# Kernel tuning notes

Measured on AMD Instinct MI355X. Metric: run time of the kernel, lower is better.

Reference implementation:

```python
import jax, jax.numpy as jnp
import numpy as np

N, F, C, E = 1024, 64, 4, 32768
H = 256       # MLP hidden width
C_OUT = 4     # new edge channels produced by nn_edge


def setup_inputs() -> dict:
    key = jax.random.key(0)
    ks = jax.random.split(key, 12)
    x = jax.random.normal(ks[0], (N, F), dtype=jnp.float32)
    edge_index = jax.random.randint(ks[1], (C, 2, E), 0, N)
    edge_weight = jax.random.uniform(ks[2], (C, E), dtype=jnp.float32)
    s_n1 = 1.0 / np.sqrt(C * F)
    s_n2 = 1.0 / np.sqrt(H)
    s_e1 = 1.0 / np.sqrt(C + 2 * F)
    return {
        "x": x,
        "edge_index": edge_index,
        "edge_weight": edge_weight,
        "Wn1": jax.random.normal(ks[3], (C * F, H), dtype=jnp.float32) * s_n1,
        "bn1": jnp.zeros((H,), jnp.float32),
        "Wn2": jax.random.normal(ks[4], (H, F), dtype=jnp.float32) * s_n2,
        "bn2": jnp.zeros((F,), jnp.float32),
        "We1": jax.random.normal(ks[5], (C + 2 * F, H), dtype=jnp.float32) * s_e1,
        "be1": jnp.zeros((H,), jnp.float32),
        "We2": jax.random.normal(ks[6], (H, C_OUT), dtype=jnp.float32) * s_n2,
        "be2": jnp.zeros((C_OUT,), jnp.float32),
        "eps": jnp.zeros((), jnp.float32),
    }


def reference(x, edge_index, edge_weight, Wn1, bn1, Wn2, bn2, We1, be1, We2, be2, eps):
    # ---- MCGNN: per-channel edge-weighted scatter-add aggregation ----
    def agg_one(ei, w):
        # ei: [2,E] (row0 = source j, row1 = target i); w: [E]
        msg = x[ei[0]] * w[:, None]                       # [E,F]
        return jax.ops.segment_sum(msg, ei[1], num_segments=N)  # [N,F]

    agg = jax.vmap(agg_one)(edge_index, edge_weight)      # [C,N,F]
    out_cat = agg + (1.0 + eps) * x                       # broadcast self term
    h = out_cat.transpose(1, 0, 2).reshape(N, C * F)      # [N, C*F]
    x_next = jax.nn.relu(h @ Wn1 + bn1) @ Wn2 + bn2       # [N,F]

    # ---- EDPGNN: dense adjacency per channel + broadcast x_i/x_j ----
    def dense_adj(ei, w):
        return jnp.zeros((N, N), x.dtype).at[ei[0], ei[1]].add(w)

    a = jax.vmap(dense_adj)(edge_index, edge_weight)      # [C,N,N]
    a = a.transpose(1, 2, 0)                              # [N,N,C]
    x_i = jnp.broadcast_to(x_next[:, None, :], (N, N, F))
    x_j = jnp.broadcast_to(x_next[None, :, :], (N, N, F))
    feat = jnp.concatenate([a, x_i, x_j], axis=2).reshape(N * N, C + 2 * F)
    adj_out = (jax.nn.relu(feat @ We1 + be1) @ We2 + be2).reshape(N, N, C_OUT)
    return adj_out
```

## Files before the change

kernel.cpp:

```cpp
#include <hip/hip_runtime.h>

#define NN 1024
#define FF 64
#define CC 4
#define EE 32768
#define HH 256

__global__ __launch_bounds__(256)
void k_agg_scatter(const float* __restrict__ x, const int* __restrict__ ei,
                   const float* __restrict__ ew, float* __restrict__ agg)
{
    unsigned t = blockIdx.x * 256u + threadIdx.x;
    unsigned f = t & 63u;
    unsigned e = (t >> 6) & (EE - 1u);
    unsigned c = t >> 21;
    int src = ei[c * 2 * EE + e];
    int dst = ei[c * 2 * EE + EE + e];
    float w = ew[c * EE + e];
    atomicAdd(&agg[dst * (CC * FF) + c * FF + f], x[src * FF + f] * w);
}

__global__ __launch_bounds__(256)
void k_adj_scatter(const int* __restrict__ ei, const float* __restrict__ ew,
                   float* __restrict__ adense)
{
    unsigned t = blockIdx.x * 256u + threadIdx.x;
    unsigned e = t & (EE - 1u);
    unsigned c = t >> 15;
    int i = ei[c * 2 * EE + e];
    int j = ei[c * 2 * EE + EE + e];
    float w = ew[c * EE + e];
    atomicAdd(&adense[(i * NN + j) * CC + c], w);
}

__global__ __launch_bounds__(256)
void k_node_mlp1(const float* __restrict__ agg, const float* __restrict__ x,
                 const float* __restrict__ Wn1, const float* __restrict__ bn1,
                 const float* __restrict__ epsp, float* __restrict__ hid)
{
    __shared__ float hval[4][256];
    const int tid = threadIdx.x;
    const int n0 = blockIdx.x * 4;
    const float ope = 1.0f + epsp[0];
#pragma unroll
    for (int nn = 0; nn < 4; ++nn)
        hval[nn][tid] = agg[(n0 + nn) * 256 + tid] + ope * x[(n0 + nn) * 64 + (tid & 63)];
    __syncthreads();
    float a0 = bn1[tid], a1 = a0, a2 = a0, a3 = a0;
    for (int k = 0; k < 256; ++k) {
        float w = Wn1[k * 256 + tid];
        a0 += hval[0][k] * w;
        a1 += hval[1][k] * w;
        a2 += hval[2][k] * w;
        a3 += hval[3][k] * w;
    }
    hid[(n0 + 0) * 256 + tid] = fmaxf(a0, 0.f);
    hid[(n0 + 1) * 256 + tid] = fmaxf(a1, 0.f);
    hid[(n0 + 2) * 256 + tid] = fmaxf(a2, 0.f);
    hid[(n0 + 3) * 256 + tid] = fmaxf(a3, 0.f);
}

__global__ __launch_bounds__(256)
void k_node_mlp2(const float* __restrict__ hid, const float* __restrict__ Wn2,
                 const float* __restrict__ bn2, float* __restrict__ xn)
{
    __shared__ float hl[4][256];
    const int tid = threadIdx.x;
    const int n0 = blockIdx.x * 4;
#pragma unroll
    for (int r = 0; r < 4; ++r) hl[r][tid] = hid[(n0 + r) * 256 + tid];
    __syncthreads();
    const int nn = tid >> 6, f = tid & 63;
    float acc = bn2[f];
    for (int k = 0; k < 256; ++k)
        acc += hl[nn][k] * Wn2[k * 64 + f];
    xn[(n0 + nn) * 64 + f] = acc;
}

__global__ __launch_bounds__(256)
void k_pq(const float* __restrict__ xn, const float* __restrict__ We1,
          const float* __restrict__ be1, float* __restrict__ P, float* __restrict__ Q)
{
    __shared__ float xl[4][64];
    const int tid = threadIdx.x;
    const int n0 = blockIdx.x * 4;
    xl[tid >> 6][tid & 63] = xn[n0 * 64 + tid];
    __syncthreads();
    float p0 = be1[tid], p1 = p0, p2 = p0, p3 = p0;
    float q0 = 0.f, q1 = 0.f, q2 = 0.f, q3 = 0.f;
    for (int f = 0; f < 64; ++f) {
        float wp = We1[(4 + f) * 256 + tid];
        float wq = We1[(68 + f) * 256 + tid];
        p0 += xl[0][f] * wp;  q0 += xl[0][f] * wq;
        p1 += xl[1][f] * wp;  q1 += xl[1][f] * wq;
        p2 += xl[2][f] * wp;  q2 += xl[2][f] * wq;
        p3 += xl[3][f] * wp;  q3 += xl[3][f] * wq;
    }
    P[(n0 + 0) * 256 + tid] = p0;  Q[(n0 + 0) * 256 + tid] = q0;
    P[(n0 + 1) * 256 + tid] = p1;  Q[(n0 + 1) * 256 + tid] = q1;
    P[(n0 + 2) * 256 + tid] = p2;  Q[(n0 + 2) * 256 + tid] = q2;
    P[(n0 + 3) * 256 + tid] = p3;  Q[(n0 + 3) * 256 + tid] = q3;
}

__global__ __launch_bounds__(256, 1)
void k_edge_mlp(const float* __restrict__ P, const float* __restrict__ Q,
                const float* __restrict__ adense, const float* __restrict__ We1,
                const float* __restrict__ We2, const float* __restrict__ be2,
                float* __restrict__ out)
{
    __shared__ float4 Pl[64 * 64];
    __shared__ float4 Ql[64 * 64];
    __shared__ float4 W2l[256];
    __shared__ float4 W1l[4 * 64];

    const int tid = threadIdx.x;
    const int iBase = blockIdx.y * 64;
    const int jBase = blockIdx.x * 64;

    for (int t = tid; t < 64 * 64; t += 256) {
        int row = t >> 6, q = t & 63;
        int ph = q ^ ((row >> 2) & 7);
        Pl[row * 64 + ph] = *(const float4*)(P + (iBase + row) * 256 + q * 4);
        Ql[row * 64 + ph] = *(const float4*)(Q + (jBase + row) * 256 + q * 4);
    }
    {
        int c = tid >> 6, q = tid & 63;
        W2l[tid] = *(const float4*)(We2 + tid * 4);
        W1l[tid] = *(const float4*)(We1 + c * 256 + q * 4);
    }
    __syncthreads();

    const int tx = tid & 15, ty = tid >> 4;
    const int ps = ty & 7, qs = tx & 7;

    float4 a[4][4];
#pragma unroll
    for (int ii = 0; ii < 4; ++ii)
#pragma unroll
        for (int jj = 0; jj < 4; ++jj)
            a[ii][jj] = *(const float4*)(adense +
                ((size_t)(iBase + ty * 4 + ii) * NN + (jBase + tx * 4 + jj)) * 4);

    float4 acc[4][4];
#pragma unroll
    for (int ii = 0; ii < 4; ++ii)
#pragma unroll
        for (int jj = 0; jj < 4; ++jj)
            acc[ii][jj] = make_float4(0.f, 0.f, 0.f, 0.f);

    for (int q = 0; q < 64; ++q) {
        float4 p[4], qv[4], w2[4], w1[4];
#pragma unroll
        for (int r = 0; r < 4; ++r) p[r]  = Pl[(ty * 4 + r) * 64 + (q ^ ps)];
#pragma unroll
        for (int r = 0; r < 4; ++r) qv[r] = Ql[(tx * 4 + r) * 64 + (q ^ qs)];
#pragma unroll
        for (int k = 0; k < 4; ++k) w2[k] = W2l[q * 4 + k];
#pragma unroll
        for (int c = 0; c < 4; ++c) w1[c] = W1l[c * 64 + q];

#pragma unroll
        for (int ii = 0; ii < 4; ++ii) {
#pragma unroll
            for (int jj = 0; jj < 4; ++jj) {
                const float4 av = a[ii][jj];
                float s0 = av.x * w1[0].x + av.y * w1[1].x + av.z * w1[2].x + av.w * w1[3].x;
                float s1 = av.x * w1[0].y + av.y * w1[1].y + av.z * w1[2].y + av.w * w1[3].y;
                float s2 = av.x * w1[0].z + av.y * w1[1].z + av.z * w1[2].z + av.w * w1[3].z;
                float s3 = av.x * w1[0].w + av.y * w1[1].w + av.z * w1[2].w + av.w * w1[3].w;
                float v0 = fmaxf(p[ii].x + qv[jj].x + s0, 0.f);
                float v1 = fmaxf(p[ii].y + qv[jj].y + s1, 0.f);
                float v2 = fmaxf(p[ii].z + qv[jj].z + s2, 0.f);
                float v3 = fmaxf(p[ii].w + qv[jj].w + s3, 0.f);
                acc[ii][jj].x += v0 * w2[0].x + v1 * w2[1].x + v2 * w2[2].x + v3 * w2[3].x;
                acc[ii][jj].y += v0 * w2[0].y + v1 * w2[1].y + v2 * w2[2].y + v3 * w2[3].y;
                acc[ii][jj].z += v0 * w2[0].z + v1 * w2[1].z + v2 * w2[2].z + v3 * w2[3].z;
                acc[ii][jj].w += v0 * w2[0].w + v1 * w2[1].w + v2 * w2[2].w + v3 * w2[3].w;
            }
        }
    }

    const float4 b2 = *(const float4*)be2;
#pragma unroll
    for (int ii = 0; ii < 4; ++ii) {
#pragma unroll
        for (int jj = 0; jj < 4; ++jj) {
            float4 o = acc[ii][jj];
            o.x += b2.x; o.y += b2.y; o.z += b2.z; o.w += b2.w;
            *(float4*)(out + ((size_t)(iBase + ty * 4 + ii) * NN + (jBase + tx * 4 + jj)) * 4) = o;
        }
    }
}

extern "C" void kernel_launch(void* const* d_in, const int* in_sizes, int n_in,
                              void* d_out, int out_size, void* d_ws, size_t ws_size,
                              hipStream_t stream)
{
    (void)in_sizes; (void)n_in; (void)out_size; (void)ws_size;
    const float* x   = (const float*)d_in[0];
    const int*   ei  = (const int*)d_in[1];
    const float* ew  = (const float*)d_in[2];
    const float* Wn1 = (const float*)d_in[3];
    const float* bn1 = (const float*)d_in[4];
    const float* Wn2 = (const float*)d_in[5];
    const float* bn2 = (const float*)d_in[6];
    const float* We1 = (const float*)d_in[7];
    const float* be1 = (const float*)d_in[8];
    const float* We2 = (const float*)d_in[9];
    const float* be2 = (const float*)d_in[10];
    const float* eps = (const float*)d_in[11];
    float* out = (float*)d_out;

    float* ws = (float*)d_ws;
    float* agg    = ws;
    float* adense = ws + 262144;
    float* hid    = ws + 4456448;
    float* xn     = ws + 4718592;
    float* Pb     = ws + 4784128;
    float* Qb     = ws + 5046272;

    hipMemsetAsync(d_ws, 0, (size_t)(262144 + 4194304) * sizeof(float), stream);

    k_agg_scatter<<<(CC * EE * FF) / 256, 256, 0, stream>>>(x, ei, ew, agg);
    k_adj_scatter<<<(CC * EE) / 256, 256, 0, stream>>>(ei, ew, adense);
    k_node_mlp1<<<NN / 4, 256, 0, stream>>>(agg, x, Wn1, bn1, eps, hid);
    k_node_mlp2<<<NN / 4, 256, 0, stream>>>(hid, Wn2, bn2, xn);
    k_pq<<<NN / 4, 256, 0, stream>>>(xn, We1, be1, Pb, Qb);

    dim3 g(NN / 64, NN / 64);
    k_edge_mlp<<<g, 256, 0, stream>>>(Pb, Qb, adense, We1, We2, be2, out);
}
```

Measured before the change: 256.4 us.

## Replace atomic scatter with counting-sort gather; retile edge MLP for occupancy

Node aggregation drops the per-feature atomic scatter in favour of a count, scan and bucket pass that sorts edges by (channel, destination), followed by an atomic-free gather per destination. The edge MLP moves from 64x64 tiles holding the full hidden dimension in LDS to 32x32 tiles that stream the hidden dimension in four chunks, which cuts LDS and register use so several blocks fit per CU. The node MLP and PQ kernels are re-threaded to compute one row per thread with larger blocks. The cost is extra launches, a single-block scan, and repeated syncs inside the edge kernel.

```diff
diff --git a/kernel.cpp b/kernel.cpp
--- a/kernel.cpp
+++ b/kernel.cpp
@@ -6,18 +6,82 @@
 #define EE 32768
 #define HH 256
 
-__global__ __launch_bounds__(256)
-void k_agg_scatter(const float* __restrict__ x, const int* __restrict__ ei,
-                   const float* __restrict__ ew, float* __restrict__ agg)
+#define OFF_ADENSE 0u
+#define OFF_CNT    4194304u
+#define OFF_OFFS   4198400u
+#define OFF_CURSOR 4202512u
+#define OFF_SRTS   4206608u
+#define OFF_SRTW   4337680u
+#define OFF_AGG    4468752u
+#define OFF_HID    4194304u
+#define OFF_XN     4730896u
+#define OFF_P      4796432u
+#define OFF_Q      5058576u
+
+__global__ __launch_bounds__(256)
+void k_count(const int* __restrict__ ei, int* __restrict__ cnt)
 {
     unsigned t = blockIdx.x * 256u + threadIdx.x;
-    unsigned f = t & 63u;
-    unsigned e = (t >> 6) & (EE - 1u);
-    unsigned c = t >> 21;
+    unsigned e = t & (EE - 1u);
+    unsigned c = t >> 15;
+    int dst = ei[c * 2 * EE + EE + e];
+    atomicAdd(&cnt[c * NN + dst], 1);
+}
+
+__global__ __launch_bounds__(1024)
+void k_scan(const int* __restrict__ cnt, int* __restrict__ offs, int* __restrict__ cursor)
+{
+    __shared__ int sums[1024];
+    const int t = threadIdx.x;
+    int c0 = cnt[t * 4], c1 = cnt[t * 4 + 1], c2 = cnt[t * 4 + 2], c3 = cnt[t * 4 + 3];
+    int s = c0 + c1 + c2 + c3;
+    sums[t] = s;
+    __syncthreads();
+    for (int d = 1; d < 1024; d <<= 1) {
+        int v = (t >= d) ? sums[t - d] : 0;
+        __syncthreads();
+        sums[t] += v;
+        __syncthreads();
+    }
+    int base = sums[t] - s;
+    offs[t * 4]     = base;           cursor[t * 4]     = base;
+    offs[t * 4 + 1] = base + c0;      cursor[t * 4 + 1] = base + c0;
+    offs[t * 4 + 2] = base + c0 + c1; cursor[t * 4 + 2] = base + c0 + c1;
+    offs[t * 4 + 3] = base + c0 + c1 + c2; cursor[t * 4 + 3] = base + c0 + c1 + c2;
+    if (t == 1023) offs[4096] = sums[1023];
+}
+
+__global__ __launch_bounds__(256)
+void k_bucket(const int* __restrict__ ei, const float* __restrict__ ew,
+              int* __restrict__ cursor, int* __restrict__ srt_src, float* __restrict__ srt_w)
+{
+    unsigned t = blockIdx.x * 256u + threadIdx.x;
+    unsigned e = t & (EE - 1u);
+    unsigned c = t >> 15;
     int src = ei[c * 2 * EE + e];
     int dst = ei[c * 2 * EE + EE + e];
     float w = ew[c * EE + e];
-    atomicAdd(&agg[dst * (CC * FF) + c * FF + f], x[src * FF + f] * w);
+    int pos = atomicAdd(&cursor[c * NN + dst], 1);
+    srt_src[pos] = src;
+    srt_w[pos] = w;
+}
+
+__global__ __launch_bounds__(256)
+void k_agg_gather(const float* __restrict__ x, const int* __restrict__ offs,
+                  const int* __restrict__ srt_src, const float* __restrict__ srt_w,
+                  float* __restrict__ agg)
+{
+    const int g = blockIdx.x * 4 + (threadIdx.x >> 6);
+    const int lane = threadIdx.x & 63;
+    const int c = g >> 10, dst = g & 1023;
+    const int beg = offs[g], end = offs[g + 1];
+    float acc = 0.f;
+    for (int k = beg; k < end; ++k) {
+        int src = srt_src[k];
+        float w = srt_w[k];
+        acc += x[src * FF + lane] * w;
+    }
+    agg[dst * (CC * FF) + c * FF + lane] = acc;
 }
 
 __global__ __launch_bounds__(256)
@@ -33,163 +97,151 @@
     atomicAdd(&adense[(i * NN + j) * CC + c], w);
 }
 
-__global__ __launch_bounds__(256)
+__global__ __launch_bounds__(1024)
 void k_node_mlp1(const float* __restrict__ agg, const float* __restrict__ x,
                  const float* __restrict__ Wn1, const float* __restrict__ bn1,
                  const float* __restrict__ epsp, float* __restrict__ hid)
 {
     __shared__ float hval[4][256];
     const int tid = threadIdx.x;
+    const int nn = tid >> 8, h = tid & 255;
     const int n0 = blockIdx.x * 4;
     const float ope = 1.0f + epsp[0];
-#pragma unroll
-    for (int nn = 0; nn < 4; ++nn)
-        hval[nn][tid] = agg[(n0 + nn) * 256 + tid] + ope * x[(n0 + nn) * 64 + (tid & 63)];
-    __syncthreads();
-    float a0 = bn1[tid], a1 = a0, a2 = a0, a3 = a0;
-    for (int k = 0; k < 256; ++k) {
-        float w = Wn1[k * 256 + tid];
-        a0 += hval[0][k] * w;
-        a1 += hval[1][k] * w;
-        a2 += hval[2][k] * w;
-        a3 += hval[3][k] * w;
-    }
-    hid[(n0 + 0) * 256 + tid] = fmaxf(a0, 0.f);
-    hid[(n0 + 1) * 256 + tid] = fmaxf(a1, 0.f);
-    hid[(n0 + 2) * 256 + tid] = fmaxf(a2, 0.f);
-    hid[(n0 + 3) * 256 + tid] = fmaxf(a3, 0.f);
-}
-
-__global__ __launch_bounds__(256)
+    hval[nn][h] = agg[(n0 + nn) * 256 + h] + ope * x[(n0 + nn) * 64 + (h & 63)];
+    __syncthreads();
+    float acc = bn1[h];
+#pragma unroll 8
+    for (int k = 0; k < 256; ++k)
+        acc += hval[nn][k] * Wn1[k * 256 + h];
+    hid[(n0 + nn) * 256 + h] = fmaxf(acc, 0.f);
+}
+
+__global__ __launch_bounds__(512)
 void k_node_mlp2(const float* __restrict__ hid, const float* __restrict__ Wn2,
                  const float* __restrict__ bn2, float* __restrict__ xn)
 {
-    __shared__ float hl[4][256];
-    const int tid = threadIdx.x;
-    const int n0 = blockIdx.x * 4;
-#pragma unroll
-    for (int r = 0; r < 4; ++r) hl[r][tid] = hid[(n0 + r) * 256 + tid];
+    __shared__ float hl[8][256];
+    const int tid = threadIdx.x;
+    const int n0 = blockIdx.x * 8;
+    for (int u = tid; u < 2048; u += 512) hl[u >> 8][u & 255] = hid[n0 * 256 + u];
     __syncthreads();
     const int nn = tid >> 6, f = tid & 63;
     float acc = bn2[f];
+#pragma unroll 8
     for (int k = 0; k < 256; ++k)
         acc += hl[nn][k] * Wn2[k * 64 + f];
     xn[(n0 + nn) * 64 + f] = acc;
 }
 
-__global__ __launch_bounds__(256)
+__global__ __launch_bounds__(1024)
 void k_pq(const float* __restrict__ xn, const float* __restrict__ We1,
           const float* __restrict__ be1, float* __restrict__ P, float* __restrict__ Q)
 {
     __shared__ float xl[4][64];
     const int tid = threadIdx.x;
+    const int r = tid >> 8, h = tid & 255;
     const int n0 = blockIdx.x * 4;
-    xl[tid >> 6][tid & 63] = xn[n0 * 64 + tid];
-    __syncthreads();
-    float p0 = be1[tid], p1 = p0, p2 = p0, p3 = p0;
-    float q0 = 0.f, q1 = 0.f, q2 = 0.f, q3 = 0.f;
+    if (tid < 256) xl[tid >> 6][tid & 63] = xn[n0 * 64 + tid];
+    __syncthreads();
+    float p = be1[h], q = 0.f;
+#pragma unroll 8
     for (int f = 0; f < 64; ++f) {
-        float wp = We1[(4 + f) * 256 + tid];
-        float wq = We1[(68 + f) * 256 + tid];
-        p0 += xl[0][f] * wp;  q0 += xl[0][f] * wq;
-        p1 += xl[1][f] * wp;  q1 += xl[1][f] * wq;
-        p2 += xl[2][f] * wp;  q2 += xl[2][f] * wq;
-        p3 += xl[3][f] * wp;  q3 += xl[3][f] * wq;
-    }
-    P[(n0 + 0) * 256 + tid] = p0;  Q[(n0 + 0) * 256 + tid] = q0;
-    P[(n0 + 1) * 256 + tid] = p1;  Q[(n0 + 1) * 256 + tid] = q1;
-    P[(n0 + 2) * 256 + tid] = p2;  Q[(n0 + 2) * 256 + tid] = q2;
-    P[(n0 + 3) * 256 + tid] = p3;  Q[(n0 + 3) * 256 + tid] = q3;
-}
-
-__global__ __launch_bounds__(256, 1)
+        float xv = xl[r][f];
+        p += xv * We1[(4 + f) * 256 + h];
+        q += xv * We1[(68 + f) * 256 + h];
+    }
+    P[(n0 + r) * 256 + h] = p;
+    Q[(n0 + r) * 256 + h] = q;
+}
+
+__global__ __launch_bounds__(256, 4)
 void k_edge_mlp(const float* __restrict__ P, const float* __restrict__ Q,
                 const float* __restrict__ adense, const float* __restrict__ We1,
                 const float* __restrict__ We2, const float* __restrict__ be2,
                 float* __restrict__ out)
 {
-    __shared__ float4 Pl[64 * 64];
-    __shared__ float4 Ql[64 * 64];
-    __shared__ float4 W2l[256];
-    __shared__ float4 W1l[4 * 64];
-
-    const int tid = threadIdx.x;
-    const int iBase = blockIdx.y * 64;
-    const int jBase = blockIdx.x * 64;
-
-    for (int t = tid; t < 64 * 64; t += 256) {
-        int row = t >> 6, q = t & 63;
-        int ph = q ^ ((row >> 2) & 7);
-        Pl[row * 64 + ph] = *(const float4*)(P + (iBase + row) * 256 + q * 4);
-        Ql[row * 64 + ph] = *(const float4*)(Q + (jBase + row) * 256 + q * 4);
-    }
-    {
-        int c = tid >> 6, q = tid & 63;
-        W2l[tid] = *(const float4*)(We2 + tid * 4);
-        W1l[tid] = *(const float4*)(We1 + c * 256 + q * 4);
-    }
-    __syncthreads();
-
+    __shared__ float4 Pl[32 * 16];
+    __shared__ float4 Ql[32 * 16];
+    __shared__ float4 W1l[4 * 16];
+    __shared__ float4 W2l[64];
+
+    const int tid = threadIdx.x;
     const int tx = tid & 15, ty = tid >> 4;
-    const int ps = ty & 7, qs = tx & 7;
-
-    float4 a[4][4];
-#pragma unroll
-    for (int ii = 0; ii < 4; ++ii)
-#pragma unroll
-        for (int jj = 0; jj < 4; ++jj)
+    const int iBase = blockIdx.y * 32, jBase = blockIdx.x * 32;
+    const int psw = ty & 7;
+    const int qsw = tx & 7;
+
+    float4 a[2][2], acc[2][2];
+#pragma unroll
+    for (int ii = 0; ii < 2; ++ii)
+#pragma unroll
+        for (int jj = 0; jj < 2; ++jj) {
             a[ii][jj] = *(const float4*)(adense +
-                ((size_t)(iBase + ty * 4 + ii) * NN + (jBase + tx * 4 + jj)) * 4);
-
-    float4 acc[4][4];
-#pragma unroll
-    for (int ii = 0; ii < 4; ++ii)
-#pragma unroll
-        for (int jj = 0; jj < 4; ++jj)
+                ((size_t)(iBase + ty * 2 + ii) * NN + (jBase + tx * 2 + jj)) * 4);
             acc[ii][jj] = make_float4(0.f, 0.f, 0.f, 0.f);
-
-    for (int q = 0; q < 64; ++q) {
-        float4 p[4], qv[4], w2[4], w1[4];
-#pragma unroll
-        for (int r = 0; r < 4; ++r) p[r]  = Pl[(ty * 4 + r) * 64 + (q ^ ps)];
-#pragma unroll
-        for (int r = 0; r < 4; ++r) qv[r] = Ql[(tx * 4 + r) * 64 + (q ^ qs)];
-#pragma unroll
-        for (int k = 0; k < 4; ++k) w2[k] = W2l[q * 4 + k];
-#pragma unroll
-        for (int c = 0; c < 4; ++c) w1[c] = W1l[c * 64 + q];
-
-#pragma unroll
-        for (int ii = 0; ii < 4; ++ii) {
-#pragma unroll
-            for (int jj = 0; jj < 4; ++jj) {
-                const float4 av = a[ii][jj];
-                float s0 = av.x * w1[0].x + av.y * w1[1].x + av.z * w1[2].x + av.w * w1[3].x;
-                float s1 = av.x * w1[0].y + av.y * w1[1].y + av.z * w1[2].y + av.w * w1[3].y;
-                float s2 = av.x * w1[0].z + av.y * w1[1].z + av.z * w1[2].z + av.w * w1[3].z;
-                float s3 = av.x * w1[0].w + av.y * w1[1].w + av.z * w1[2].w + av.w * w1[3].w;
-                float v0 = fmaxf(p[ii].x + qv[jj].x + s0, 0.f);
-                float v1 = fmaxf(p[ii].y + qv[jj].y + s1, 0.f);
-                float v2 = fmaxf(p[ii].z + qv[jj].z + s2, 0.f);
-                float v3 = fmaxf(p[ii].w + qv[jj].w + s3, 0.f);
-                acc[ii][jj].x += v0 * w2[0].x + v1 * w2[1].x + v2 * w2[2].x + v3 * w2[3].x;
-                acc[ii][jj].y += v0 * w2[0].y + v1 * w2[1].y + v2 * w2[2].y + v3 * w2[3].y;
-                acc[ii][jj].z += v0 * w2[0].z + v1 * w2[1].z + v2 * w2[2].z + v3 * w2[3].z;
-                acc[ii][jj].w += v0 * w2[0].w + v1 * w2[1].w + v2 * w2[2].w + v3 * w2[3].w;
+        }
+
+    for (int hc = 0; hc < 4; ++hc) {
+        __syncthreads();
+#pragma unroll
+        for (int u = 0; u < 2; ++u) {
+            int idx = tid + u * 256;
+            int row = idx >> 4, q = idx & 15;
+            int ph = q ^ ((row >> 1) & 7);
+            Pl[row * 16 + ph] = *(const float4*)(P + (iBase + row) * 256 + hc * 64 + q * 4);
+            Ql[row * 16 + ph] = *(const float4*)(Q + (jBase + row) * 256 + hc * 64 + q * 4);
+        }
+        if (tid < 64) {
+            int c = tid >> 4, q = tid & 15;
+            W1l[tid] = *(const float4*)(We1 + c * 256 + hc * 64 + q * 4);
+        } else if (tid < 128) {
+            int h = tid - 64;
+            W2l[h] = *(const float4*)(We2 + (hc * 64 + h) * 4);
+        }
+        __syncthreads();
+
+        for (int q = 0; q < 16; ++q) {
+            float4 p[2], qv[2], w1[4], w2[4];
+#pragma unroll
+            for (int r = 0; r < 2; ++r) p[r]  = Pl[(ty * 2 + r) * 16 + (q ^ psw)];
+#pragma unroll
+            for (int r = 0; r < 2; ++r) qv[r] = Ql[(tx * 2 + r) * 16 + (q ^ qsw)];
+#pragma unroll
+            for (int c = 0; c < 4; ++c) w1[c] = W1l[c * 16 + q];
+#pragma unroll
+            for (int k = 0; k < 4; ++k) w2[k] = W2l[q * 4 + k];
+
+#pragma unroll
+            for (int ii = 0; ii < 2; ++ii) {
+#pragma unroll
+                for (int jj = 0; jj < 2; ++jj) {
+                    const float4 av = a[ii][jj];
+                    float s0 = av.x * w1[0].x + av.y * w1[1].x + av.z * w1[2].x + av.w * w1[3].x;
+                    float s1 = av.x * w1[0].y + av.y * w1[1].y + av.z * w1[2].y + av.w * w1[3].y;
+                    float s2 = av.x * w1[0].z + av.y * w1[1].z + av.z * w1[2].z + av.w * w1[3].z;
+                    float s3 = av.x * w1[0].w + av.y * w1[1].w + av.z * w1[2].w + av.w * w1[3].w;
+                    float v0 = fmaxf(p[ii].x + qv[jj].x + s0, 0.f);
+                    float v1 = fmaxf(p[ii].y + qv[jj].y + s1, 0.f);
+                    float v2 = fmaxf(p[ii].z + qv[jj].z + s2, 0.f);
+                    float v3 = fmaxf(p[ii].w + qv[jj].w + s3, 0.f);
+                    acc[ii][jj].x += v0 * w2[0].x + v1 * w2[1].x + v2 * w2[2].x + v3 * w2[3].x;
+                    acc[ii][jj].y += v0 * w2[0].y + v1 * w2[1].y + v2 * w2[2].y + v3 * w2[3].y;
+                    acc[ii][jj].z += v0 * w2[0].z + v1 * w2[1].z + v2 * w2[2].z + v3 * w2[3].z;
+                    acc[ii][jj].w += v0 * w2[0].w + v1 * w2[1].w + v2 * w2[2].w + v3 * w2[3].w;
+                }
             }
         }
     }
 
     const float4 b2 = *(const float4*)be2;
 #pragma unroll
-    for (int ii = 0; ii < 4; ++ii) {
-#pragma unroll
-        for (int jj = 0; jj < 4; ++jj) {
+    for (int ii = 0; ii < 2; ++ii)
+#pragma unroll
+        for (int jj = 0; jj < 2; ++jj) {
             float4 o = acc[ii][jj];
             o.x += b2.x; o.y += b2.y; o.z += b2.z; o.w += b2.w;
-            *(float4*)(out + ((size_t)(iBase + ty * 4 + ii) * NN + (jBase + tx * 4 + jj)) * 4) = o;
-        }
-    }
+            *(float4*)(out + ((size_t)(iBase + ty * 2 + ii) * NN + (jBase + tx * 2 + jj)) * 4) = o;
+        }
 }
 
 extern "C" void kernel_launch(void* const* d_in, const int* in_sizes, int n_in,
@@ -212,21 +264,29 @@
     float* out = (float*)d_out;
 
     float* ws = (float*)d_ws;
-    float* agg    = ws;
-    float* adense = ws + 262144;
-    float* hid    = ws + 4456448;
-    float* xn     = ws + 4718592;
-    float* Pb     = ws + 4784128;
-    float* Qb     = ws + 5046272;
-
-    hipMemsetAsync(d_ws, 0, (size_t)(262144 + 4194304) * sizeof(float), stream);
-
-    k_agg_scatter<<<(CC * EE * FF) / 256, 256, 0, stream>>>(x, ei, ew, agg);
+    float* adense = ws + OFF_ADENSE;
+    int*   cnt    = (int*)(ws + OFF_CNT);
+    int*   offs   = (int*)(ws + OFF_OFFS);
+    int*   cursor = (int*)(ws + OFF_CURSOR);
+    int*   srts   = (int*)(ws + OFF_SRTS);
+    float* srtw   = ws + OFF_SRTW;
+    float* agg    = ws + OFF_AGG;
+    float* hid    = ws + OFF_HID;
+    float* xn     = ws + OFF_XN;
+    float* Pb     = ws + OFF_P;
+    float* Qb     = ws + OFF_Q;
+
+    hipMemsetAsync(d_ws, 0, (size_t)(4194304 + 4096) * sizeof(float), stream);
+
+    k_count      <<<(CC * EE) / 256, 256, 0, stream>>>(ei, cnt);
+    k_scan       <<<1, 1024, 0, stream>>>(cnt, offs, cursor);
+    k_bucket     <<<(CC * EE) / 256, 256, 0, stream>>>(ei, ew, cursor, srts, srtw);
     k_adj_scatter<<<(CC * EE) / 256, 256, 0, stream>>>(ei, ew, adense);
-    k_node_mlp1<<<NN / 4, 256, 0, stream>>>(agg, x, Wn1, bn1, eps, hid);
-    k_node_mlp2<<<NN / 4, 256, 0, stream>>>(hid, Wn2, bn2, xn);
-    k_pq<<<NN / 4, 256, 0, stream>>>(xn, We1, be1, Pb, Qb);
-
-    dim3 g(NN / 64, NN / 64);
+    k_agg_gather <<<(CC * NN) / 4, 256, 0, stream>>>(x, offs, srts, srtw, agg);
+    k_node_mlp1  <<<NN / 4, 1024, 0, stream>>>(agg, x, Wn1, bn1, eps, hid);
+    k_node_mlp2  <<<NN / 8, 512, 0, stream>>>(hid, Wn2, bn2, xn);
+    k_pq         <<<NN / 4, 1024, 0, stream>>>(xn, We1, be1, Pb, Qb);
+
+    dim3 g(NN / 32, NN / 32);
     k_edge_mlp<<<g, 256, 0, stream>>>(Pb, Qb, adense, We1, We2, be2, out);
 }
```

After: 257.5 us. About the same (+0.4%).
